# Kernel tuning notes

Measured on AMD Instinct MI355X. Metric: run time of the kernel, lower is better.

## Reference

```python
import jax, jax.numpy as jnp
import numpy as np

B, L, F_OP, F_EU, D, H = 4, 512, 10, 2, 128, 128


def setup_inputs() -> dict:
    key = jax.random.key(0)
    ks = jax.random.split(key, 16)

    def lin_w(k, fin, fout):
        # kaiming-ish init, stored [in, out] so forward is x @ W + b
        return (jax.random.normal(k, (fin, fout), jnp.float32) * (1.0 / np.sqrt(fin)))

    return {
        "inputs": jax.random.normal(ks[0], (B, L, F_OP), jnp.float32),
        "coords": jax.random.normal(ks[1], (B, L, F_EU), jnp.float32),
        "targets": jax.random.normal(ks[2], (B, L, 1), jnp.float32),
        "cc": jax.random.normal(ks[3], (B, L, F_EU), jnp.float32),
        # all sequences fully occupied -> static shapes everywhere
        "input_lenths": jnp.full((B,), L, dtype=jnp.int32),
        "Wc": lin_w(ks[4], F_OP + F_EU, D), "bc": jnp.zeros((D,), jnp.float32),
        "Wcc": lin_w(ks[5], F_OP + F_EU, D), "bcc": jnp.zeros((D,), jnp.float32),
        "Wa": lin_w(ks[6], D, D), "ba": jnp.zeros((D,), jnp.float32),
        "Wb": lin_w(ks[7], D, D), "bb": jnp.zeros((D,), jnp.float32),
        # GraphSAGE layer 1 (SAGEConv: lin_l on mean-aggregated msgs w/ bias, lin_r on root, no bias)
        "W1l": lin_w(ks[8], D, H), "b1l": jnp.zeros((H,), jnp.float32),
        "W1r": lin_w(ks[9], D, H),
        # GraphSAGE layer 2 -> scalar output
        "W2l": lin_w(ks[10], H, 1), "b2l": jnp.zeros((1,), jnp.float32),
        "W2r": lin_w(ks[11], H, 1),
    }


def _forward(inputs, coords, targets, cc,
             Wc, bc, Wcc, bcc, Wa, ba, Wb, bb,
             W1l, b1l, W1r, W2l, b2l, W2r):
    b_, l_, _ = inputs.shape
    d = Wa.shape[0]
    scale = 1.0 / np.sqrt(d)

    inputs_c = inputs - inputs[:, 0:1, :]
    i_emb = jnp.concatenate([inputs, coords], axis=-1) @ Wc + bc      # [B,L,D]
    ic_emb = jnp.concatenate([inputs_c, cc], axis=-1) @ Wcc + bcc     # [B,L,D]

    a = i_emb @ Wa + ba
    bt = i_emb @ Wb + bb
    a_c = ic_emb @ Wa + ba
    b_c = ic_emb @ Wb + bb

    adj = jnp.einsum('bid,bjd->bij', a, bt) * scale       # [B,L,L]
    adj_c = jnp.einsum('bid,bjd->bij', a_c, b_c) * scale

    # full lengths -> softmax_mask all False; MSE over the full matrices
    diff = jnp.mean((adj - adj_c) ** 2)

    # eval mode, full lengths: adj_mat_inplace has -inf only on the diagonal,
    # so exactly one entry per row is invalid after topk(k=L); the surviving
    # edges are the top (L-1) entries of adj per row (the row minimum drops).
    _, top_idx = jax.lax.top_k(adj, l_)                   # [B,L,L] descending
    src_local = top_idx[:, :, : l_ - 1]                   # [B,L,L-1]

    offsets = (jnp.arange(b_, dtype=jnp.int32) * l_)[:, None, None]
    src = (src_local.astype(jnp.int32) + offsets).reshape(-1)          # edge sources
    tgt = jnp.broadcast_to(jnp.arange(l_, dtype=jnp.int32)[None, :, None] + offsets,
                           (b_, l_, l_ - 1)).reshape(-1)               # edge targets

    x = (i_emb - ic_emb).reshape(b_ * l_, d)              # node features [N,D]
    n_nodes = b_ * l_
    deg = jnp.float32(l_ - 1)                             # every node has L-1 in-edges

    def sage_conv(h, Wl, bl, Wr):
        agg = jax.ops.segment_sum(h[src], tgt, num_segments=n_nodes) / deg
        return agg @ Wl + bl + h @ Wr

    h1 = jax.nn.relu(sage_conv(x, W1l, b1l, W1r))         # [N,H]
    out = sage_conv(h1, W2l, b2l, W2r)                    # [N,1]

    out_head = out.reshape(b_, l_, 1)[:, 0]               # first node per sample [B,1]
    target_head = targets[:, 0]                           # [B,1]
    return out_head, diff, target_head


def reference(inputs, coords, targets, cc, input_lenths,
              Wc, bc, Wcc, bcc, Wa, ba, Wb, bb,
              W1l, b1l, W1r, W2l, b2l, W2r):
    # input_lenths are all == L (full sequences) so masks are static no-ops.
    return _forward(inputs, coords, targets, cc,
                    Wc, bc, Wcc, bcc, Wa, ba, Wb, bb,
                    W1l, b1l, W1r, W2l, b2l, W2r)
```

## Files before the change

### kernel.cpp

```cpp
#include <hip/hip_runtime.h>
#include <math.h>

#define BB 4
#define LL 512
#define NROW (BB*LL)
#define DD 128
#define DEG 511.0f
#define SCALE 0.08838834764831845f

typedef short bf16x8 __attribute__((ext_vector_type(8)));
typedef float f32x4 __attribute__((ext_vector_type(4)));

static __device__ __forceinline__ ushort f2bf(float f) {
  unsigned u = __float_as_uint(f);
  u = (u + 0x7fffu + ((u >> 16) & 1u)) >> 16;
  return (ushort)u;
}

__global__ __launch_bounds__(256) void k_front(
    const float* __restrict__ inputs, const float* __restrict__ coords,
    const float* __restrict__ cc,
    const float* __restrict__ Wc, const float* __restrict__ bc,
    const float* __restrict__ Wcc, const float* __restrict__ bcc,
    const float* __restrict__ Wa, const float* __restrict__ ba,
    const float* __restrict__ Wb, const float* __restrict__ bb,
    const float* __restrict__ W1l, const float* __restrict__ W1r,
    ushort* __restrict__ bfA, ushort* __restrict__ bfB,
    ushort* __restrict__ bfAc, ushort* __restrict__ bfBc,
    float* __restrict__ P, float* __restrict__ Q,
    float* __restrict__ xpart) {
  int bx = blockIdx.x, m = blockIdx.y;
  int t = threadIdx.x;
  int row0 = bx * 16;
  int b = bx >> 5;
  __shared__ float fin1[16][12], fin2[16][12];
  __shared__ float Es[16][132];
  __shared__ float cs[2][128];
  if (t < 192) {
    int r = t / 12, k = t % 12;
    int row = row0 + r;
    float v1, v2;
    if (k < 10) {
      float v = inputs[row*10 + k];
      v1 = v;
      v2 = v - inputs[(b*LL)*10 + k];
    } else {
      v1 = coords[row*2 + (k-10)];
      v2 = cc[row*2 + (k-10)];
    }
    fin1[r][k] = v1;
    fin2[r][k] = v2;
  }
  __syncthreads();
  for (int it = 0; it < 8; ++it) {
    int idx = t + it*256;
    int r = idx >> 7, d = idx & 127;
    float e;
    if (m == 0) {
      e = bc[d];
#pragma unroll
      for (int k = 0; k < 12; ++k) e += fin1[r][k] * Wc[k*DD + d];
    } else if (m == 1) {
      e = bcc[d];
#pragma unroll
      for (int k = 0; k < 12; ++k) e += fin2[r][k] * Wcc[k*DD + d];
    } else {
      float e1 = bc[d], e2 = bcc[d];
#pragma unroll
      for (int k = 0; k < 12; ++k) {
        e1 += fin1[r][k] * Wc[k*DD + d];
        e2 += fin2[r][k] * Wcc[k*DD + d];
      }
      e = e1 - e2;
    }
    Es[r][d] = e;
  }
  __syncthreads();
  if (m == 2) {
    int d = t & 127, h = t >> 7;
    float s = 0.f;
#pragma unroll
    for (int r = 0; r < 8; ++r) s += Es[h*8 + r][d];
    cs[h][d] = s;
    __syncthreads();
    if (h == 0) xpart[bx*DD + d] = cs[0][d] + cs[1][d];
  }
  const float* U = (m == 2) ? W1l : Wa;
  const float* V = (m == 2) ? W1r : Wb;
  int tx = t & 31, ty = t >> 5;
  int d0 = tx*4, r0 = ty*2;
  float aU0[4]={0,0,0,0}, aU1[4]={0,0,0,0}, aV0[4]={0,0,0,0}, aV1[4]={0,0,0,0};
#pragma unroll 4
  for (int k = 0; k < DD; ++k) {
    float4 u = *(const float4*)&U[k*DD + d0];
    float4 v = *(const float4*)&V[k*DD + d0];
    float e0 = Es[r0][k], e1 = Es[r0+1][k];
    aU0[0]+=e0*u.x; aU0[1]+=e0*u.y; aU0[2]+=e0*u.z; aU0[3]+=e0*u.w;
    aU1[0]+=e1*u.x; aU1[1]+=e1*u.y; aU1[2]+=e1*u.z; aU1[3]+=e1*u.w;
    aV0[0]+=e0*v.x; aV0[1]+=e0*v.y; aV0[2]+=e0*v.z; aV0[3]+=e0*v.w;
    aV1[0]+=e1*v.x; aV1[1]+=e1*v.y; aV1[2]+=e1*v.z; aV1[3]+=e1*v.w;
  }
  if (m < 2) {
    float4 bu = *(const float4*)&ba[d0];
    float4 bw = *(const float4*)&bb[d0];
    ushort* dU = (m == 0) ? bfA : bfAc;
    ushort* dV = (m == 0) ? bfB : bfBc;
    ushort4 o;
    o = make_ushort4(f2bf(aU0[0]+bu.x), f2bf(aU0[1]+bu.y), f2bf(aU0[2]+bu.z), f2bf(aU0[3]+bu.w));
    *(ushort4*)&dU[(row0+r0)*DD + d0] = o;
    o = make_ushort4(f2bf(aU1[0]+bu.x), f2bf(aU1[1]+bu.y), f2bf(aU1[2]+bu.z), f2bf(aU1[3]+bu.w));
    *(ushort4*)&dU[(row0+r0+1)*DD + d0] = o;
    o = make_ushort4(f2bf(aV0[0]+bw.x), f2bf(aV0[1]+bw.y), f2bf(aV0[2]+bw.z), f2bf(aV0[3]+bw.w));
    *(ushort4*)&dV[(row0+r0)*DD + d0] = o;
    o = make_ushort4(f2bf(aV1[0]+bw.x), f2bf(aV1[1]+bw.y), f2bf(aV1[2]+bw.z), f2bf(aV1[3]+bw.w));
    *(ushort4*)&dV[(row0+r0+1)*DD + d0] = o;
  } else {
    *(float4*)&P[(row0+r0)*DD + d0]   = make_float4(aU0[0],aU0[1],aU0[2],aU0[3]);
    *(float4*)&P[(row0+r0+1)*DD + d0] = make_float4(aU1[0],aU1[1],aU1[2],aU1[3]);
    *(float4*)&Q[(row0+r0)*DD + d0]   = make_float4(aV0[0],aV0[1],aV0[2],aV0[3]);
    *(float4*)&Q[(row0+r0+1)*DD + d0] = make_float4(aV1[0],aV1[1],aV1[2],aV1[3]);
  }
}

__global__ __launch_bounds__(256) void k_adj(
    const ushort* __restrict__ bfA, const ushort* __restrict__ bfB,
    const ushort* __restrict__ bfAc, const ushort* __restrict__ bfBc,
    float* __restrict__ diffpart, float* __restrict__ minval, int* __restrict__ minidx) {
  __shared__ ushort Bs[64][136], Bcs[64][136];
  __shared__ float red[256];
  int t = threadIdx.x;
  int ix = blockIdx.x, jy = blockIdx.y, b = blockIdx.z;
  int i0 = b*LL + ix*64, j0 = b*LL + jy*64;
  int wave = t >> 6, lane = t & 63;
  int rowA = i0 + wave*16 + (lane & 15);
  int koff = (lane >> 4) * 8;
  bf16x8 av[4], acv[4];
#pragma unroll
  for (int ks = 0; ks < 4; ++ks) {
    av[ks]  = *(const bf16x8*)&bfA[(size_t)rowA*DD + ks*32 + koff];
    acv[ks] = *(const bf16x8*)&bfAc[(size_t)rowA*DD + ks*32 + koff];
  }
  for (int it = 0; it < 4; ++it) {
    int chunk = t + it*256;
    int row = chunk >> 4, c4 = chunk & 15;
    *(uint4*)&Bs[row][c4*8]  = *(const uint4*)&bfB[(size_t)(j0+row)*DD + c4*8];
    *(uint4*)&Bcs[row][c4*8] = *(const uint4*)&bfBc[(size_t)(j0+row)*DD + c4*8];
  }
  __syncthreads();
  f32x4 zf = {0.f, 0.f, 0.f, 0.f};
  f32x4 acc[4], accc[4];
#pragma unroll
  for (int jt = 0; jt < 4; ++jt) { acc[jt] = zf; accc[jt] = zf; }
#pragma unroll
  for (int ks = 0; ks < 4; ++ks) {
#pragma unroll
    for (int jt = 0; jt < 4; ++jt) {
      bf16x8 bv  = *(const bf16x8*)&Bs[jt*16 + (lane&15)][ks*32 + koff];
      bf16x8 bcv = *(const bf16x8*)&Bcs[jt*16 + (lane&15)][ks*32 + koff];
      acc[jt]  = __builtin_amdgcn_mfma_f32_16x16x32_bf16(av[ks],  bv,  acc[jt],  0,0,0);
      accc[jt] = __builtin_amdgcn_mfma_f32_16x16x32_bf16(acv[ks], bcv, accc[jt], 0,0,0);
    }
  }
  int g = lane >> 4, c = lane & 15;
  float sq = 0.f;
#pragma unroll
  for (int r = 0; r < 4; ++r) {
    float mn = INFINITY; int mi = -1;
#pragma unroll
    for (int jt = 0; jt < 4; ++jt) {
      float v  = acc[jt][r]  * SCALE;
      float vc = accc[jt][r] * SCALE;
      float d = v - vc;
      sq += d*d;
      int j = j0 + jt*16 + c;
      if (v < mn || (v == mn && j > mi)) { mn = v; mi = j; }
    }
#pragma unroll
    for (int msk = 1; msk < 16; msk <<= 1) {
      float ov = __shfl_xor(mn, msk);
      int   oi = __shfl_xor(mi, msk);
      if (ov < mn || (ov == mn && oi > mi)) { mn = ov; mi = oi; }
    }
    if (c == 0) {
      int gi = i0 + wave*16 + g*4 + r;
      minval[gi*8 + jy] = mn;
      minidx[gi*8 + jy] = mi;
    }
  }
  red[t] = sq;
  __syncthreads();
  for (int off = 128; off > 0; off >>= 1) {
    if (t < off) red[t] += red[t+off];
    __syncthreads();
  }
  if (t == 0) diffpart[(b*8 + jy)*8 + ix] = red[0];
}

__global__ __launch_bounds__(1024) void k_tail(
    const float* __restrict__ P, const float* __restrict__ Q,
    const float* __restrict__ xpart, const float* __restrict__ W1l,
    const float* __restrict__ b1l,
    const float* __restrict__ minval, const int* __restrict__ minidx,
    const float* __restrict__ diffpart, const float* __restrict__ targets,
    const float* __restrict__ W2l, const float* __restrict__ b2l,
    const float* __restrict__ W2r, float* __restrict__ out) {
  int b = blockIdx.x, t = threadIdx.x;
  int d = t & 127, h = t >> 7;
  __shared__ int aminL[LL];
  __shared__ float part[8][128];
  __shared__ float xs[128];
  __shared__ float sbv[128];
  if (t < LL) {
    int row = b*LL + t;
    float mv = minval[row*8]; int mi = minidx[row*8];
#pragma unroll
    for (int ch = 1; ch < 8; ++ch) {
      float v = minval[row*8 + ch]; int i2 = minidx[row*8 + ch];
      if (v < mv || (v == mv && i2 > mi)) { mv = v; mi = i2; }
    }
    aminL[t] = mi;
  }
  float s = 0.f;
#pragma unroll
  for (int i = h; i < 32; i += 8) s += xpart[(b*32 + i)*DD + d];
  part[h][d] = s;
  __syncthreads();
  if (h == 0) {
    float v = 0.f;
#pragma unroll
    for (int q = 0; q < 8; ++q) v += part[q][d];
    xs[d] = v;
  }
  __syncthreads();
  float acc = 0.f;
#pragma unroll
  for (int k = h*16; k < h*16 + 16; ++k) acc += xs[k] * W1l[k*DD + d];
  part[h][d] = acc;
  __syncthreads();
  if (h == 0) {
    float v = 0.f;
#pragma unroll
    for (int q = 0; q < 8; ++q) v += part[q][d];
    sbv[d] = v;
  }
  __syncthreads();
  float base = sbv[d] * (1.0f/DEG) + b1l[d];
  float csum = 0.f;
  int l0 = h*64;
#pragma unroll 4
  for (int r = 0; r < 64; ++r) {
    int li = l0 + r;
    int am = aminL[li];
    float v = base - P[(size_t)am*DD + d] * (1.0f/DEG) + Q[(size_t)(b*LL + li)*DD + d];
    csum += fmaxf(v, 0.f);
  }
  part[h][d] = csum;
  __syncthreads();
  if (h == 0) {
    float colsum = 0.f;
#pragma unroll
    for (int q = 0; q < 8; ++q) colsum += part[q][d];
    int amh = aminL[0];
    int am2 = aminL[amh - b*LL];
    float h1head = fmaxf(base - P[(size_t)amh*DD + d]*(1.0f/DEG) + Q[(size_t)(b*LL)*DD + d], 0.f);
    float h1am   = fmaxf(base - P[(size_t)am2*DD + d]*(1.0f/DEG) + Q[(size_t)amh*DD + d], 0.f);
    float agg = (colsum - h1am) * (1.0f/DEG);
    part[0][d] = agg * W2l[d] + h1head * W2r[d];
  }
  __syncthreads();
  if (t < 64) {
    float v = part[0][t] + part[0][t + 64];
#pragma unroll
    for (int msk = 32; msk > 0; msk >>= 1) v += __shfl_down(v, msk);
    if (t == 0) out[b] = v + b2l[0];
  }
  if (b == 0) {
    __shared__ float dred[256];
    if (t < 256) dred[t] = diffpart[t];
    __syncthreads();
    for (int off = 128; off > 0; off >>= 1) {
      if (t < off) dred[t] += dred[t+off];
      __syncthreads();
    }
    if (t == 0) out[4] = dred[0] / (float)((float)BB*LL*LL);
    if (t < 4) out[5+t] = targets[t*LL];
  }
}

extern "C" void kernel_launch(void* const* d_in, const int* in_sizes, int n_in,
                              void* d_out, int out_size, void* d_ws, size_t ws_size,
                              hipStream_t stream) {
  const float* inputs  = (const float*)d_in[0];
  const float* coords  = (const float*)d_in[1];
  const float* targets = (const float*)d_in[2];
  const float* cc      = (const float*)d_in[3];
  const float* Wc  = (const float*)d_in[5];
  const float* bc  = (const float*)d_in[6];
  const float* Wcc = (const float*)d_in[7];
  const float* bcc = (const float*)d_in[8];
  const float* Wa  = (const float*)d_in[9];
  const float* ba  = (const float*)d_in[10];
  const float* Wb  = (const float*)d_in[11];
  const float* bb  = (const float*)d_in[12];
  const float* W1l = (const float*)d_in[13];
  const float* b1l = (const float*)d_in[14];
  const float* W1r = (const float*)d_in[15];
  const float* W2l = (const float*)d_in[16];
  const float* b2l = (const float*)d_in[17];
  const float* W2r = (const float*)d_in[18];
  float* out = (float*)d_out;

  float* ws = (float*)d_ws;
  float* P  = ws;
  float* Q  = ws + (size_t)NROW*DD;
  ushort* bfA  = (ushort*)(ws + (size_t)2*NROW*DD);
  ushort* bfB  = bfA  + (size_t)NROW*DD;
  ushort* bfAc = bfB  + (size_t)NROW*DD;
  ushort* bfBc = bfAc + (size_t)NROW*DD;
  float* xpart    = ws + (size_t)4*NROW*DD;
  float* diffpart = xpart + 128*DD;
  float* minval   = diffpart + 256;
  int*   minidx   = (int*)(minval + (size_t)NROW*8);

  k_front<<<dim3(128, 3), 256, 0, stream>>>(inputs, coords, cc, Wc, bc, Wcc, bcc,
                                            Wa, ba, Wb, bb, W1l, W1r,
                                            bfA, bfB, bfAc, bfBc, P, Q, xpart);
  k_adj  <<<dim3(8, 8, 4), 256, 0, stream>>>(bfA, bfB, bfAc, bfBc, diffpart, minval, minidx);
  k_tail <<<4, 1024, 0, stream>>>(P, Q, xpart, W1l, b1l, minval, minidx, diffpart, targets,
                                  W2l, b2l, W2r, out);
}
```

Before: 46.18 us.

## Fuse embedding projection into adjacency tiles and move GNN projections into tail kernel

Removes the separate front kernel. Each adjacency block now recomputes the input embeddings and the Wa/Wb projections for its own 64 row and 64 column tiles using MFMA, keeping them in shared memory. The tail kernel computes x, P and Q itself with MFMA over 4 blocks. This cuts one launch and the global round trip of the bf16 intermediates, but adds redundant recomputation across 64 blocks per batch, per-block weight transposes, larger shared memory use, and serial work in a 4-block tail.

```diff
diff --git a/kernel.cpp b/kernel.cpp
--- a/kernel.cpp
+++ b/kernel.cpp
@@ -17,137 +17,102 @@
   return (ushort)u;
 }
 
-__global__ __launch_bounds__(256) void k_front(
+__global__ __launch_bounds__(256) void k_fused(
     const float* __restrict__ inputs, const float* __restrict__ coords,
     const float* __restrict__ cc,
     const float* __restrict__ Wc, const float* __restrict__ bc,
     const float* __restrict__ Wcc, const float* __restrict__ bcc,
     const float* __restrict__ Wa, const float* __restrict__ ba,
     const float* __restrict__ Wb, const float* __restrict__ bb,
-    const float* __restrict__ W1l, const float* __restrict__ W1r,
-    ushort* __restrict__ bfA, ushort* __restrict__ bfB,
-    ushort* __restrict__ bfAc, ushort* __restrict__ bfBc,
-    float* __restrict__ P, float* __restrict__ Q,
-    float* __restrict__ xpart) {
-  int bx = blockIdx.x, m = blockIdx.y;
-  int t = threadIdx.x;
-  int row0 = bx * 16;
-  int b = bx >> 5;
-  __shared__ float fin1[16][12], fin2[16][12];
-  __shared__ float Es[16][132];
-  __shared__ float cs[2][128];
-  if (t < 192) {
-    int r = t / 12, k = t % 12;
-    int row = row0 + r;
-    float v1, v2;
-    if (k < 10) {
-      float v = inputs[row*10 + k];
-      v1 = v;
-      v2 = v - inputs[(b*LL)*10 + k];
-    } else {
-      v1 = coords[row*2 + (k-10)];
-      v2 = cc[row*2 + (k-10)];
-    }
-    fin1[r][k] = v1;
-    fin2[r][k] = v2;
-  }
-  __syncthreads();
-  for (int it = 0; it < 8; ++it) {
-    int idx = t + it*256;
-    int r = idx >> 7, d = idx & 127;
-    float e;
-    if (m == 0) {
-      e = bc[d];
-#pragma unroll
-      for (int k = 0; k < 12; ++k) e += fin1[r][k] * Wc[k*DD + d];
-    } else if (m == 1) {
-      e = bcc[d];
-#pragma unroll
-      for (int k = 0; k < 12; ++k) e += fin2[r][k] * Wcc[k*DD + d];
-    } else {
-      float e1 = bc[d], e2 = bcc[d];
-#pragma unroll
-      for (int k = 0; k < 12; ++k) {
-        e1 += fin1[r][k] * Wc[k*DD + d];
-        e2 += fin2[r][k] * Wcc[k*DD + d];
-      }
-      e = e1 - e2;
-    }
-    Es[r][d] = e;
-  }
-  __syncthreads();
-  if (m == 2) {
-    int d = t & 127, h = t >> 7;
-    float s = 0.f;
-#pragma unroll
-    for (int r = 0; r < 8; ++r) s += Es[h*8 + r][d];
-    cs[h][d] = s;
-    __syncthreads();
-    if (h == 0) xpart[bx*DD + d] = cs[0][d] + cs[1][d];
-  }
-  const float* U = (m == 2) ? W1l : Wa;
-  const float* V = (m == 2) ? W1r : Wb;
-  int tx = t & 31, ty = t >> 5;
-  int d0 = tx*4, r0 = ty*2;
-  float aU0[4]={0,0,0,0}, aU1[4]={0,0,0,0}, aV0[4]={0,0,0,0}, aV1[4]={0,0,0,0};
-#pragma unroll 4
-  for (int k = 0; k < DD; ++k) {
-    float4 u = *(const float4*)&U[k*DD + d0];
-    float4 v = *(const float4*)&V[k*DD + d0];
-    float e0 = Es[r0][k], e1 = Es[r0+1][k];
-    aU0[0]+=e0*u.x; aU0[1]+=e0*u.y; aU0[2]+=e0*u.z; aU0[3]+=e0*u.w;
-    aU1[0]+=e1*u.x; aU1[1]+=e1*u.y; aU1[2]+=e1*u.z; aU1[3]+=e1*u.w;
-    aV0[0]+=e0*v.x; aV0[1]+=e0*v.y; aV0[2]+=e0*v.z; aV0[3]+=e0*v.w;
-    aV1[0]+=e1*v.x; aV1[1]+=e1*v.y; aV1[2]+=e1*v.z; aV1[3]+=e1*v.w;
-  }
-  if (m < 2) {
-    float4 bu = *(const float4*)&ba[d0];
-    float4 bw = *(const float4*)&bb[d0];
-    ushort* dU = (m == 0) ? bfA : bfAc;
-    ushort* dV = (m == 0) ? bfB : bfBc;
-    ushort4 o;
-    o = make_ushort4(f2bf(aU0[0]+bu.x), f2bf(aU0[1]+bu.y), f2bf(aU0[2]+bu.z), f2bf(aU0[3]+bu.w));
-    *(ushort4*)&dU[(row0+r0)*DD + d0] = o;
-    o = make_ushort4(f2bf(aU1[0]+bu.x), f2bf(aU1[1]+bu.y), f2bf(aU1[2]+bu.z), f2bf(aU1[3]+bu.w));
-    *(ushort4*)&dU[(row0+r0+1)*DD + d0] = o;
-    o = make_ushort4(f2bf(aV0[0]+bw.x), f2bf(aV0[1]+bw.y), f2bf(aV0[2]+bw.z), f2bf(aV0[3]+bw.w));
-    *(ushort4*)&dV[(row0+r0)*DD + d0] = o;
-    o = make_ushort4(f2bf(aV1[0]+bw.x), f2bf(aV1[1]+bw.y), f2bf(aV1[2]+bw.z), f2bf(aV1[3]+bw.w));
-    *(ushort4*)&dV[(row0+r0+1)*DD + d0] = o;
-  } else {
-    *(float4*)&P[(row0+r0)*DD + d0]   = make_float4(aU0[0],aU0[1],aU0[2],aU0[3]);
-    *(float4*)&P[(row0+r0+1)*DD + d0] = make_float4(aU1[0],aU1[1],aU1[2],aU1[3]);
-    *(float4*)&Q[(row0+r0)*DD + d0]   = make_float4(aV0[0],aV0[1],aV0[2],aV0[3]);
-    *(float4*)&Q[(row0+r0+1)*DD + d0] = make_float4(aV1[0],aV1[1],aV1[2],aV1[3]);
-  }
-}
-
-__global__ __launch_bounds__(256) void k_adj(
-    const ushort* __restrict__ bfA, const ushort* __restrict__ bfB,
-    const ushort* __restrict__ bfAc, const ushort* __restrict__ bfBc,
     float* __restrict__ diffpart, float* __restrict__ minval, int* __restrict__ minidx) {
-  __shared__ ushort Bs[64][136], Bcs[64][136];
+  __shared__ ushort E1[64][136], E2[64][136];
+  __shared__ ushort aT[64][136], acT[64][136], bT[64][136], bcT[64][136];
+  __shared__ float bcS[128], bccS[128], biasS[128], headIn[12];
   __shared__ float red[256];
+  __shared__ __align__(16) char uni[34816];
+  float (*fin1)[12] = (float(*)[12])uni;
+  float (*fin2)[12] = (float(*)[12])(uni + 3072);
+  ushort (*WT)[136] = (ushort(*)[136])uni;
+
   int t = threadIdx.x;
   int ix = blockIdx.x, jy = blockIdx.y, b = blockIdx.z;
   int i0 = b*LL + ix*64, j0 = b*LL + jy*64;
-  int wave = t >> 6, lane = t & 63;
-  int rowA = i0 + wave*16 + (lane & 15);
-  int koff = (lane >> 4) * 8;
+  int lane = t & 63, wave = t >> 6;
+  int d = t & 127;
+
+  if (t < 128) { bcS[t] = bc[t]; bccS[t] = bcc[t]; }
+  if (t < 12)  headIn[t] = (t < 10) ? inputs[(size_t)(b*LL)*10 + t] : 0.f;
+  float wcR[12], wccR[12];
+#pragma unroll
+  for (int k = 0; k < 12; ++k) { wcR[k] = Wc[k*DD + d]; wccR[k] = Wcc[k*DD + d]; }
+  __syncthreads();
+
+  for (int side = 0; side < 2; ++side) {
+    int rows0 = side ? j0 : i0;
+    const float* W    = side ? Wb : Wa;
+    const float* bias = side ? bb : ba;
+    for (int idx = t; idx < 768; idx += 256) {
+      int r = idx / 12, k = idx - r*12;
+      int grow = rows0 + r;
+      float f1, f2;
+      if (k < 10) { float v = inputs[(size_t)grow*10 + k]; f1 = v; f2 = v - headIn[k]; }
+      else        { f1 = coords[(size_t)grow*2 + (k-10)]; f2 = cc[(size_t)grow*2 + (k-10)]; }
+      fin1[r][k] = f1; fin2[r][k] = f2;
+    }
+    __syncthreads();
+    {
+      int r0 = t >> 7;
+      for (int it = 0; it < 32; ++it) {
+        int r = r0 + it*2;
+        float e1 = bcS[d], e2 = bccS[d];
+#pragma unroll
+        for (int k = 0; k < 12; ++k) { e1 += fin1[r][k]*wcR[k]; e2 += fin2[r][k]*wccR[k]; }
+        E1[r][d] = f2bf(e1); E2[r][d] = f2bf(e2);
+      }
+    }
+    __syncthreads();
+    for (int idx = t; idx < 16384; idx += 256) {
+      int kk = idx >> 7, dd = idx & 127;
+      WT[dd][kk] = f2bf(W[idx]);
+    }
+    if (t < 128) biasS[t] = bias[t];
+    __syncthreads();
+    {
+      ushort (*o1)[136] = side ? bT : aT;
+      ushort (*o2)[136] = side ? bcT : acT;
+      int rloc = lane & 15, koff = (lane >> 4)*8;
+      int rbase = wave*16;
+      for (int ct = 0; ct < 8; ++ct) {
+        f32x4 p1 = {0.f,0.f,0.f,0.f}, p2 = {0.f,0.f,0.f,0.f};
+#pragma unroll
+        for (int ks = 0; ks < 4; ++ks) {
+          bf16x8 ef1 = *(const bf16x8*)&E1[rbase + rloc][ks*32 + koff];
+          bf16x8 ef2 = *(const bf16x8*)&E2[rbase + rloc][ks*32 + koff];
+          bf16x8 wf  = *(const bf16x8*)&WT[ct*16 + rloc][ks*32 + koff];
+          p1 = __builtin_amdgcn_mfma_f32_16x16x32_bf16(ef1, wf, p1, 0,0,0);
+          p2 = __builtin_amdgcn_mfma_f32_16x16x32_bf16(ef2, wf, p2, 0,0,0);
+        }
+        int col = ct*16 + rloc;
+        float bv = biasS[col];
+#pragma unroll
+        for (int r = 0; r < 4; ++r) {
+          int row = rbase + (lane>>4)*4 + r;
+          o1[row][col] = f2bf(p1[r] + bv);
+          o2[row][col] = f2bf(p2[r] + bv);
+        }
+      }
+    }
+    __syncthreads();
+  }
+
+  int rloc = lane & 15, koff = (lane >> 4)*8;
   bf16x8 av[4], acv[4];
 #pragma unroll
   for (int ks = 0; ks < 4; ++ks) {
-    av[ks]  = *(const bf16x8*)&bfA[(size_t)rowA*DD + ks*32 + koff];
-    acv[ks] = *(const bf16x8*)&bfAc[(size_t)rowA*DD + ks*32 + koff];
-  }
-  for (int it = 0; it < 4; ++it) {
-    int chunk = t + it*256;
-    int row = chunk >> 4, c4 = chunk & 15;
-    *(uint4*)&Bs[row][c4*8]  = *(const uint4*)&bfB[(size_t)(j0+row)*DD + c4*8];
-    *(uint4*)&Bcs[row][c4*8] = *(const uint4*)&bfBc[(size_t)(j0+row)*DD + c4*8];
-  }
-  __syncthreads();
-  f32x4 zf = {0.f, 0.f, 0.f, 0.f};
+    av[ks]  = *(const bf16x8*)&aT[wave*16 + rloc][ks*32 + koff];
+    acv[ks] = *(const bf16x8*)&acT[wave*16 + rloc][ks*32 + koff];
+  }
+  f32x4 zf = {0.f,0.f,0.f,0.f};
   f32x4 acc[4], accc[4];
 #pragma unroll
   for (int jt = 0; jt < 4; ++jt) { acc[jt] = zf; accc[jt] = zf; }
@@ -155,8 +120,8 @@
   for (int ks = 0; ks < 4; ++ks) {
 #pragma unroll
     for (int jt = 0; jt < 4; ++jt) {
-      bf16x8 bv  = *(const bf16x8*)&Bs[jt*16 + (lane&15)][ks*32 + koff];
-      bf16x8 bcv = *(const bf16x8*)&Bcs[jt*16 + (lane&15)][ks*32 + koff];
+      bf16x8 bv  = *(const bf16x8*)&bT[jt*16 + rloc][ks*32 + koff];
+      bf16x8 bcv = *(const bf16x8*)&bcT[jt*16 + rloc][ks*32 + koff];
       acc[jt]  = __builtin_amdgcn_mfma_f32_16x16x32_bf16(av[ks],  bv,  acc[jt],  0,0,0);
       accc[jt] = __builtin_amdgcn_mfma_f32_16x16x32_bf16(acv[ks], bcv, accc[jt], 0,0,0);
     }
@@ -170,8 +135,8 @@
     for (int jt = 0; jt < 4; ++jt) {
       float v  = acc[jt][r]  * SCALE;
       float vc = accc[jt][r] * SCALE;
-      float d = v - vc;
-      sq += d*d;
+      float dd = v - vc;
+      sq += dd*dd;
       int j = j0 + jt*16 + c;
       if (v < mn || (v == mn && j > mi)) { mn = v; mi = j; }
     }
@@ -196,20 +161,90 @@
   if (t == 0) diffpart[(b*8 + jy)*8 + ix] = red[0];
 }
 
-__global__ __launch_bounds__(1024) void k_tail(
-    const float* __restrict__ P, const float* __restrict__ Q,
-    const float* __restrict__ xpart, const float* __restrict__ W1l,
-    const float* __restrict__ b1l,
+__global__ __launch_bounds__(1024) void k_tail2(
+    const float* __restrict__ inputs, const float* __restrict__ coords,
+    const float* __restrict__ cc,
+    const float* __restrict__ Wc, const float* __restrict__ bc,
+    const float* __restrict__ Wcc, const float* __restrict__ bcc,
+    const float* __restrict__ W1l, const float* __restrict__ b1l,
+    const float* __restrict__ W1r,
     const float* __restrict__ minval, const int* __restrict__ minidx,
     const float* __restrict__ diffpart, const float* __restrict__ targets,
     const float* __restrict__ W2l, const float* __restrict__ b2l,
-    const float* __restrict__ W2r, float* __restrict__ out) {
+    const float* __restrict__ W2r,
+    float* __restrict__ Pg, float* __restrict__ Qg, float* __restrict__ out) {
+  __shared__ ushort W1lT[128][136], W1rT[128][136];
+  __shared__ ushort xT[128][136];
+  __shared__ float finC1[128][12], finC2[128][12];
+  __shared__ float dbcS[128], headIn[12];
+  __shared__ float xs[128], sbv[128];
+  __shared__ float part[8][128];
+  __shared__ int aminL[LL];
+  __shared__ float dred[256];
+
   int b = blockIdx.x, t = threadIdx.x;
   int d = t & 127, h = t >> 7;
-  __shared__ int aminL[LL];
-  __shared__ float part[8][128];
-  __shared__ float xs[128];
-  __shared__ float sbv[128];
+  int lane = t & 63;
+
+  for (int idx = t; idx < 16384; idx += 1024) {
+    int kk = idx >> 7, dd = idx & 127;
+    W1lT[dd][kk] = f2bf(W1l[idx]);
+    W1rT[dd][kk] = f2bf(W1r[idx]);
+  }
+  if (t < 128) dbcS[t] = bc[t] - bcc[t];
+  if (t < 12)  headIn[t] = (t < 10) ? inputs[(size_t)(b*LL)*10 + t] : 0.f;
+  float wcR[12], wccR[12];
+#pragma unroll
+  for (int k = 0; k < 12; ++k) { wcR[k] = Wc[k*DD + d]; wccR[k] = Wcc[k*DD + d]; }
+
+  float csx = 0.f;
+  for (int cch = 0; cch < 4; ++cch) {
+    int rows0 = b*LL + cch*128;
+    __syncthreads();
+    for (int idx = t; idx < 1536; idx += 1024) {
+      int r = idx / 12, k = idx - r*12;
+      int grow = rows0 + r;
+      float f1, f2;
+      if (k < 10) { float v = inputs[(size_t)grow*10 + k]; f1 = v; f2 = v - headIn[k]; }
+      else        { f1 = coords[(size_t)grow*2 + (k-10)]; f2 = cc[(size_t)grow*2 + (k-10)]; }
+      finC1[r][k] = f1; finC2[r][k] = f2;
+    }
+    __syncthreads();
+    for (int rr = 0; rr < 16; ++rr) {
+      int r = h*16 + rr;
+      float xv = dbcS[d];
+#pragma unroll
+      for (int k = 0; k < 12; ++k) xv += finC1[r][k]*wcR[k] - finC2[r][k]*wccR[k];
+      xT[r][d] = f2bf(xv);
+      csx += xv;
+    }
+    __syncthreads();
+    {
+      int w = t >> 6;
+      int rg = w & 7, mat = w >> 3;
+      int rloc = lane & 15, koff = (lane >> 4)*8;
+      const ushort (*WTp)[136] = mat ? W1rT : W1lT;
+      float* dst = mat ? Qg : Pg;
+      for (int ct = 0; ct < 8; ++ct) {
+        f32x4 p = {0.f,0.f,0.f,0.f};
+#pragma unroll
+        for (int ks = 0; ks < 4; ++ks) {
+          bf16x8 af = *(const bf16x8*)&xT[rg*16 + rloc][ks*32 + koff];
+          bf16x8 wf = *(const bf16x8*)&WTp[ct*16 + rloc][ks*32 + koff];
+          p = __builtin_amdgcn_mfma_f32_16x16x32_bf16(af, wf, p, 0,0,0);
+        }
+        int col = ct*16 + rloc;
+#pragma unroll
+        for (int r = 0; r < 4; ++r) {
+          int grow = rows0 + rg*16 + (lane>>4)*4 + r;
+          dst[(size_t)grow*DD + col] = p[r];
+        }
+      }
+    }
+  }
+  __syncthreads();
+
+  part[h][d] = csx;
   if (t < LL) {
     int row = b*LL + t;
     float mv = minval[row*8]; int mi = minidx[row*8];
@@ -220,10 +255,6 @@
     }
     aminL[t] = mi;
   }
-  float s = 0.f;
-#pragma unroll
-  for (int i = h; i < 32; i += 8) s += xpart[(b*32 + i)*DD + d];
-  part[h][d] = s;
   __syncthreads();
   if (h == 0) {
     float v = 0.f;
@@ -232,10 +263,12 @@
     xs[d] = v;
   }
   __syncthreads();
-  float acc = 0.f;
-#pragma unroll
-  for (int k = h*16; k < h*16 + 16; ++k) acc += xs[k] * W1l[k*DD + d];
-  part[h][d] = acc;
+  {
+    float acc = 0.f;
+#pragma unroll
+    for (int k = h*16; k < h*16 + 16; ++k) acc += xs[k] * W1l[k*DD + d];
+    part[h][d] = acc;
+  }
   __syncthreads();
   if (h == 0) {
     float v = 0.f;
@@ -251,7 +284,7 @@
   for (int r = 0; r < 64; ++r) {
     int li = l0 + r;
     int am = aminL[li];
-    float v = base - P[(size_t)am*DD + d] * (1.0f/DEG) + Q[(size_t)(b*LL + li)*DD + d];
+    float v = base - Pg[(size_t)am*DD + d] * (1.0f/DEG) + Qg[(size_t)(b*LL + li)*DD + d];
     csum += fmaxf(v, 0.f);
   }
   part[h][d] = csum;
@@ -262,8 +295,8 @@
     for (int q = 0; q < 8; ++q) colsum += part[q][d];
     int amh = aminL[0];
     int am2 = aminL[amh - b*LL];
-    float h1head = fmaxf(base - P[(size_t)amh*DD + d]*(1.0f/DEG) + Q[(size_t)(b*LL)*DD + d], 0.f);
-    float h1am   = fmaxf(base - P[(size_t)am2*DD + d]*(1.0f/DEG) + Q[(size_t)amh*DD + d], 0.f);
+    float h1head = fmaxf(base - Pg[(size_t)amh*DD + d]*(1.0f/DEG) + Qg[(size_t)(b*LL)*DD + d], 0.f);
+    float h1am   = fmaxf(base - Pg[(size_t)am2*DD + d]*(1.0f/DEG) + Qg[(size_t)amh*DD + d], 0.f);
     float agg = (colsum - h1am) * (1.0f/DEG);
     part[0][d] = agg * W2l[d] + h1head * W2r[d];
   }
@@ -275,7 +308,6 @@
     if (t == 0) out[b] = v + b2l[0];
   }
   if (b == 0) {
-    __shared__ float dred[256];
     if (t < 256) dred[t] = diffpart[t];
     __syncthreads();
     for (int off = 128; off > 0; off >>= 1) {
@@ -311,21 +343,15 @@
   float* out = (float*)d_out;
 
   float* ws = (float*)d_ws;
-  float* P  = ws;
-  float* Q  = ws + (size_t)NROW*DD;
-  ushort* bfA  = (ushort*)(ws + (size_t)2*NROW*DD);
-  ushort* bfB  = bfA  + (size_t)NROW*DD;
-  ushort* bfAc = bfB  + (size_t)NROW*DD;
-  ushort* bfBc = bfAc + (size_t)NROW*DD;
-  float* xpart    = ws + (size_t)4*NROW*DD;
-  float* diffpart = xpart + 128*DD;
+  float* Pg = ws;
+  float* Qg = ws + (size_t)NROW*DD;
+  float* diffpart = ws + (size_t)2*NROW*DD;
   float* minval   = diffpart + 256;
   int*   minidx   = (int*)(minval + (size_t)NROW*8);
 
-  k_front<<<dim3(128, 3), 256, 0, stream>>>(inputs, coords, cc, Wc, bc, Wcc, bcc,
-                                            Wa, ba, Wb, bb, W1l, W1r,
-                                            bfA, bfB, bfAc, bfBc, P, Q, xpart);
-  k_adj  <<<dim3(8, 8, 4), 256, 0, stream>>>(bfA, bfB, bfAc, bfBc, diffpart, minval, minidx);
-  k_tail <<<4, 1024, 0, stream>>>(P, Q, xpart, W1l, b1l, minval, minidx, diffpart, targets,
-                                  W2l, b2l, W2r, out);
+  k_fused<<<dim3(8, 8, 4), 256, 0, stream>>>(inputs, coords, cc, Wc, bc, Wcc, bcc,
+                                             Wa, ba, Wb, bb, diffpart, minval, minidx);
+  k_tail2<<<4, 1024, 0, stream>>>(inputs, coords, cc, Wc, bc, Wcc, bcc,
+                                  W1l, b1l, W1r, minval, minidx, diffpart, targets,
+                                  W2l, b2l, W2r, Pg, Qg, out);
 }
```

Result: slower. 70.41 us (+52.5%).

## Spread tail GraphSAGE stage over 64 blocks with atomic output accumulation

Applied to the files above, without the earlier changes.

The tail kernel moves from 4 blocks of 1024 threads to 64 blocks of 256 threads. Each block handles 32 nodes and reduces its partial layer-2 contribution into the output with an atomicAdd. The MSE partial sums likewise go straight into the output through atomics from the adjacency kernel, and the front kernel zeroes the output and copies the targets. This spreads the latency-bound tail over more CUs and drops the diffpart buffer, but every block recomputes the W1l matvec and float summation order becomes nondeterministic.

```diff
diff --git a/kernel.cpp b/kernel.cpp
--- a/kernel.cpp
+++ b/kernel.cpp
@@ -7,6 +7,7 @@
 #define DD 128
 #define DEG 511.0f
 #define SCALE 0.08838834764831845f
+#define INVN (1.0f/((float)BB*LL*LL))
 
 typedef short bf16x8 __attribute__((ext_vector_type(8)));
 typedef float f32x4 __attribute__((ext_vector_type(4)));
@@ -19,7 +20,7 @@
 
 __global__ __launch_bounds__(256) void k_front(
     const float* __restrict__ inputs, const float* __restrict__ coords,
-    const float* __restrict__ cc,
+    const float* __restrict__ cc, const float* __restrict__ targets,
     const float* __restrict__ Wc, const float* __restrict__ bc,
     const float* __restrict__ Wcc, const float* __restrict__ bcc,
     const float* __restrict__ Wa, const float* __restrict__ ba,
@@ -28,9 +29,13 @@
     ushort* __restrict__ bfA, ushort* __restrict__ bfB,
     ushort* __restrict__ bfAc, ushort* __restrict__ bfBc,
     float* __restrict__ P, float* __restrict__ Q,
-    float* __restrict__ xpart) {
+    float* __restrict__ xpart, float* __restrict__ out) {
   int bx = blockIdx.x, m = blockIdx.y;
   int t = threadIdx.x;
+  if (m == 2 && bx == 0) {
+    if (t < 5) out[t] = 0.f;
+    if (t >= 8 && t < 12) out[5 + (t-8)] = targets[(t-8)*LL];
+  }
   int row0 = bx * 16;
   int b = bx >> 5;
   __shared__ float fin1[16][12], fin2[16][12];
@@ -125,7 +130,7 @@
 __global__ __launch_bounds__(256) void k_adj(
     const ushort* __restrict__ bfA, const ushort* __restrict__ bfB,
     const ushort* __restrict__ bfAc, const ushort* __restrict__ bfBc,
-    float* __restrict__ diffpart, float* __restrict__ minval, int* __restrict__ minidx) {
+    float* __restrict__ minval, int* __restrict__ minidx, float* __restrict__ out) {
   __shared__ ushort Bs[64][136], Bcs[64][136];
   __shared__ float red[256];
   int t = threadIdx.x;
@@ -193,25 +198,25 @@
     if (t < off) red[t] += red[t+off];
     __syncthreads();
   }
-  if (t == 0) diffpart[(b*8 + jy)*8 + ix] = red[0];
-}
-
-__global__ __launch_bounds__(1024) void k_tail(
+  if (t == 0) atomicAdd(&out[4], red[0] * INVN);
+}
+
+__global__ __launch_bounds__(256) void k_tail(
     const float* __restrict__ P, const float* __restrict__ Q,
     const float* __restrict__ xpart, const float* __restrict__ W1l,
     const float* __restrict__ b1l,
     const float* __restrict__ minval, const int* __restrict__ minidx,
-    const float* __restrict__ diffpart, const float* __restrict__ targets,
     const float* __restrict__ W2l, const float* __restrict__ b2l,
     const float* __restrict__ W2r, float* __restrict__ out) {
-  int b = blockIdx.x, t = threadIdx.x;
+  int bx = blockIdx.x, t = threadIdx.x;
+  int b = bx >> 4;
   int d = t & 127, h = t >> 7;
-  __shared__ int aminL[LL];
-  __shared__ float part[8][128];
+  __shared__ int aminL[32];
   __shared__ float xs[128];
-  __shared__ float sbv[128];
-  if (t < LL) {
-    int row = b*LL + t;
+  __shared__ float cs[2][128];
+  __shared__ float red[256];
+  if (t < 32) {
+    int row = bx*32 + t;
     float mv = minval[row*8]; int mi = minidx[row*8];
 #pragma unroll
     for (int ch = 1; ch < 8; ++ch) {
@@ -220,71 +225,53 @@
     }
     aminL[t] = mi;
   }
-  float s = 0.f;
-#pragma unroll
-  for (int i = h; i < 32; i += 8) s += xpart[(b*32 + i)*DD + d];
-  part[h][d] = s;
-  __syncthreads();
-  if (h == 0) {
-    float v = 0.f;
-#pragma unroll
-    for (int q = 0; q < 8; ++q) v += part[q][d];
-    xs[d] = v;
-  }
-  __syncthreads();
-  float acc = 0.f;
-#pragma unroll
-  for (int k = h*16; k < h*16 + 16; ++k) acc += xs[k] * W1l[k*DD + d];
-  part[h][d] = acc;
-  __syncthreads();
-  if (h == 0) {
-    float v = 0.f;
-#pragma unroll
-    for (int q = 0; q < 8; ++q) v += part[q][d];
-    sbv[d] = v;
-  }
-  __syncthreads();
-  float base = sbv[d] * (1.0f/DEG) + b1l[d];
-  float csum = 0.f;
-  int l0 = h*64;
+  {
+    float s = 0.f;
+#pragma unroll
+    for (int i = 0; i < 16; ++i) s += xpart[(b*32 + h*16 + i)*DD + d];
+    cs[h][d] = s;
+  }
+  __syncthreads();
+  if (h == 0) xs[d] = cs[0][d] + cs[1][d];
+  __syncthreads();
+  {
+    float acc = 0.f;
+    for (int k = h*64; k < h*64 + 64; ++k) acc += xs[k] * W1l[k*DD + d];
+    cs[h][d] = acc;
+  }
+  __syncthreads();
+  float sbv = cs[0][d] + cs[1][d];
+  float base = sbv * (1.0f/DEG) + b1l[d];
+  float ps = 0.f;
 #pragma unroll 4
-  for (int r = 0; r < 64; ++r) {
-    int li = l0 + r;
+  for (int rr = 0; rr < 16; ++rr) {
+    int li = h*16 + rr;
+    int i = bx*32 + li;
     int am = aminL[li];
-    float v = base - P[(size_t)am*DD + d] * (1.0f/DEG) + Q[(size_t)(b*LL + li)*DD + d];
-    csum += fmaxf(v, 0.f);
-  }
-  part[h][d] = csum;
-  __syncthreads();
-  if (h == 0) {
-    float colsum = 0.f;
-#pragma unroll
-    for (int q = 0; q < 8; ++q) colsum += part[q][d];
+    float v = base - P[(size_t)am*DD + d] * (1.0f/DEG) + Q[(size_t)i*DD + d];
+    ps += fmaxf(v, 0.f);
+  }
+  float w2l = W2l[d];
+  float contrib = ps * w2l * (1.0f/DEG);
+  if ((bx & 15) == 0 && h == 0) {
     int amh = aminL[0];
-    int am2 = aminL[amh - b*LL];
+    float mv = minval[amh*8]; int am2 = minidx[amh*8];
+#pragma unroll
+    for (int ch = 1; ch < 8; ++ch) {
+      float v = minval[amh*8 + ch]; int i2 = minidx[amh*8 + ch];
+      if (v < mv || (v == mv && i2 > am2)) { mv = v; am2 = i2; }
+    }
+    float h1amh  = fmaxf(base - P[(size_t)am2*DD + d]*(1.0f/DEG) + Q[(size_t)amh*DD + d], 0.f);
     float h1head = fmaxf(base - P[(size_t)amh*DD + d]*(1.0f/DEG) + Q[(size_t)(b*LL)*DD + d], 0.f);
-    float h1am   = fmaxf(base - P[(size_t)am2*DD + d]*(1.0f/DEG) + Q[(size_t)amh*DD + d], 0.f);
-    float agg = (colsum - h1am) * (1.0f/DEG);
-    part[0][d] = agg * W2l[d] + h1head * W2r[d];
-  }
-  __syncthreads();
-  if (t < 64) {
-    float v = part[0][t] + part[0][t + 64];
-#pragma unroll
-    for (int msk = 32; msk > 0; msk >>= 1) v += __shfl_down(v, msk);
-    if (t == 0) out[b] = v + b2l[0];
-  }
-  if (b == 0) {
-    __shared__ float dred[256];
-    if (t < 256) dred[t] = diffpart[t];
+    contrib += -h1amh * (1.0f/DEG) * w2l + h1head * W2r[d];
+  }
+  red[t] = contrib;
+  __syncthreads();
+  for (int off = 128; off > 0; off >>= 1) {
+    if (t < off) red[t] += red[t+off];
     __syncthreads();
-    for (int off = 128; off > 0; off >>= 1) {
-      if (t < off) dred[t] += dred[t+off];
-      __syncthreads();
-    }
-    if (t == 0) out[4] = dred[0] / (float)((float)BB*LL*LL);
-    if (t < 4) out[5+t] = targets[t*LL];
-  }
+  }
+  if (t == 0) atomicAdd(&out[b], red[0] + (((bx & 15) == 0) ? b2l[0] : 0.f));
 }
 
 extern "C" void kernel_launch(void* const* d_in, const int* in_sizes, int n_in,
@@ -311,21 +298,20 @@
   float* out = (float*)d_out;
 
   float* ws = (float*)d_ws;
-  float* P  = ws;
-  float* Q  = ws + (size_t)NROW*DD;
+  float* Pg = ws;
+  float* Qg = ws + (size_t)NROW*DD;
   ushort* bfA  = (ushort*)(ws + (size_t)2*NROW*DD);
   ushort* bfB  = bfA  + (size_t)NROW*DD;
   ushort* bfAc = bfB  + (size_t)NROW*DD;
   ushort* bfBc = bfAc + (size_t)NROW*DD;
-  float* xpart    = ws + (size_t)4*NROW*DD;
-  float* diffpart = xpart + 128*DD;
-  float* minval   = diffpart + 256;
-  int*   minidx   = (int*)(minval + (size_t)NROW*8);
-
-  k_front<<<dim3(128, 3), 256, 0, stream>>>(inputs, coords, cc, Wc, bc, Wcc, bcc,
+  float* xpart  = ws + (size_t)4*NROW*DD;
+  float* minval = xpart + 128*DD;
+  int*   minidx = (int*)(minval + (size_t)NROW*8);
+
+  k_front<<<dim3(128, 3), 256, 0, stream>>>(inputs, coords, cc, targets, Wc, bc, Wcc, bcc,
                                             Wa, ba, Wb, bb, W1l, W1r,
-                                            bfA, bfB, bfAc, bfBc, P, Q, xpart);
-  k_adj  <<<dim3(8, 8, 4), 256, 0, stream>>>(bfA, bfB, bfAc, bfBc, diffpart, minval, minidx);
-  k_tail <<<4, 1024, 0, stream>>>(P, Q, xpart, W1l, b1l, minval, minidx, diffpart, targets,
+                                            bfA, bfB, bfAc, bfBc, Pg, Qg, xpart, out);
+  k_adj  <<<dim3(8, 8, 4), 256, 0, stream>>>(bfA, bfB, bfAc, bfBc, minval, minidx, out);
+  k_tail <<<64, 256, 0, stream>>>(Pg, Qg, xpart, W1l, b1l, minval, minidx,
                                   W2l, b2l, W2r, out);
 }
```

Measured after the change: 42.13 us. 1.1x faster.
